# Performance work log

Hardware: AMD Instinct MI355X
Metric: run time of the kernel (lower is better)

Reference implementation:

```python
import jax, jax.numpy as jnp
import numpy as np
from jax import lax

OBS_LEN = 8; FUT_LEN = 12; NC = 2
HT = 32; HG = 32; NZ = 8
G = 1024; P = 64; N = G * P
HPRED = HT + HG + NZ  # 72


def setup_inputs() -> dict:
    key = jax.random.key(0)
    ks = jax.random.split(key, 32)
    f = lambda k, s: jax.random.normal(k, s, dtype=jnp.float32)
    p = lambda k, s: 0.1 * jax.random.normal(k, s, dtype=jnp.float32)
    inp = {
        'obs_traj_rel': f(ks[0], (OBS_LEN, N, NC + 1)),
        'z': f(ks[1], (G, NZ)),
        'traj_h0': f(ks[2], (N, HT)),
        'traj_c0': f(ks[3], (N, HT)),
        'graph_h0': f(ks[4], (N, HG)),
        'graph_c0': f(ks[5], (N, HG)),
        'w_ih_traj': p(ks[6], (4 * HT, NC + 1)),
        'w_hh_traj': p(ks[7], (4 * HT, HT)),
        'b_ih_traj': p(ks[8], (4 * HT,)),
        'b_hh_traj': p(ks[9], (4 * HT,)),
        'gat1_w': p(ks[10], (4, 32, 16)),
        'gat1_asrc': p(ks[11], (4, 16, 1)),
        'gat1_adst': p(ks[12], (4, 16, 1)),
        'gat1_b': jnp.zeros((16,), jnp.float32),
        'gat2_w': p(ks[13], (1, 64, 32)),
        'gat2_asrc': p(ks[14], (1, 32, 1)),
        'gat2_adst': p(ks[15], (1, 32, 1)),
        'gat2_b': jnp.zeros((32,), jnp.float32),
        'w_ih_graph': p(ks[16], (4 * HG, 32)),
        'w_hh_graph': p(ks[17], (4 * HG, HG)),
        'b_ih_graph': p(ks[18], (4 * HG,)),
        'b_hh_graph': p(ks[19], (4 * HG,)),
        'w_ih_pred': p(ks[20], (4 * HPRED, NC)),
        'w_hh_pred': p(ks[21], (4 * HPRED, HPRED)),
        'b_ih_pred': p(ks[22], (4 * HPRED,)),
        'b_hh_pred': p(ks[23], (4 * HPRED,)),
        'w_out': p(ks[24], (NC, HPRED)),
        'b_out': jnp.zeros((NC,), jnp.float32),
        'seq_start_end': jnp.stack([jnp.arange(G) * P, (jnp.arange(G) + 1) * P], axis=1).astype(jnp.int32),
    }
    return inp


def _lstm_cell(x, hc, w_ih, w_hh, b_ih, b_hh):
    h, c = hc
    g = x @ w_ih.T + b_ih + h @ w_hh.T + b_hh
    i, f, gg, o = jnp.split(g, 4, axis=-1)
    c2 = jax.nn.sigmoid(f) * c + jax.nn.sigmoid(i) * jnp.tanh(gg)
    h2 = jax.nn.sigmoid(o) * jnp.tanh(c2)
    return h2, c2


def _inorm(x):  # InstanceNorm1d over node axis: x [T, n, f], normalize over n
    m = x.mean(axis=1, keepdims=True)
    v = x.var(axis=1, keepdims=True)
    return (x - m) * lax.rsqrt(v + 1e-5)


def _gat_layer(x, w, a_src, a_dst, b):
    # x: [T, n, f_in], w: [H, f_in, f_out]
    hp = jnp.einsum('tnf,hfo->thno', x, w)              # [T,H,n,f_out]
    s = jnp.einsum('thno,hoi->thni', hp, a_src)[..., 0]  # [T,H,n]
    d = jnp.einsum('thno,hoi->thni', hp, a_dst)[..., 0]  # [T,H,n]
    attn = s[:, :, :, None] + d[:, :, None, :]           # [T,H,n,n]
    attn = jax.nn.softmax(jax.nn.leaky_relu(attn, 0.2), axis=-1)
    return jnp.einsum('thnm,thmo->thno', attn, hp) + b


def reference(obs_traj_rel, z, traj_h0, traj_c0, graph_h0, graph_c0,
              w_ih_traj, w_hh_traj, b_ih_traj, b_hh_traj,
              gat1_w, gat1_asrc, gat1_adst, gat1_b,
              gat2_w, gat2_asrc, gat2_adst, gat2_b,
              w_ih_graph, w_hh_graph, b_ih_graph, b_hh_graph,
              w_ih_pred, w_hh_pred, b_ih_pred, b_hh_pred,
              w_out, b_out, seq_start_end):
    n_graphs = seq_start_end.shape[0]
    n_total = obs_traj_rel.shape[1]
    peds = n_total // n_graphs  # equal-size subgraphs

    # ---- observation trajectory LSTM ----
    def traj_step(hc, x):
        hc2 = _lstm_cell(x, hc, w_ih_traj, w_hh_traj, b_ih_traj, b_hh_traj)
        return hc2, hc2[0]
    _, traj_hs = lax.scan(traj_step, (traj_h0, traj_c0), obs_traj_rel)  # [T,N,HT]

    # ---- GAT encoder per subgraph (vmapped over equal-size graphs) ----
    def gat_net(x):  # x: [T, peds, 32]
        x = _inorm(x)
        o1 = _gat_layer(x, gat1_w, gat1_asrc, gat1_adst, gat1_b)  # [T,4,n,16]
        t, h, n, fo = o1.shape
        x = jax.nn.elu(jnp.transpose(o1, (0, 2, 1, 3)).reshape(t, n, h * fo))  # [T,n,64]
        x = _inorm(x)
        o2 = _gat_layer(x, gat2_w, gat2_asrc, gat2_adst, gat2_b)  # [T,1,n,32]
        return o2[:, 0]

    xg = traj_hs.reshape(OBS_LEN, n_graphs, peds, HT)
    graph_in = jax.vmap(gat_net, in_axes=1, out_axes=1)(xg)  # [T,G,peds,32]
    graph_in = graph_in.reshape(OBS_LEN, n_total, 32)

    # ---- graph LSTM ----
    def graph_step(hc, x):
        hc2 = _lstm_cell(x, hc, w_ih_graph, w_hh_graph, b_ih_graph, b_hh_graph)
        return hc2, hc2[0]
    _, graph_hs = lax.scan(graph_step, (graph_h0, graph_c0), graph_in)

    # ---- add noise + prediction decoder (eval path, counter=True) ----
    enc = jnp.concatenate([traj_hs[-1], graph_hs[-1]], axis=1)          # [N,64]
    enc_c = jnp.concatenate([jnp.zeros_like(traj_hs[-1]), graph_hs[-1]], axis=1)
    z_rep = jnp.repeat(z, peds, axis=0)                                 # [N,8]
    h = jnp.concatenate([enc, z_rep], axis=1)                           # [N,72]
    h_c = jnp.concatenate([enc_c, z_rep], axis=1)
    c = jnp.zeros_like(h)
    c_c = jnp.zeros_like(h_c)
    out0 = obs_traj_rel[OBS_LEN - 1, :, :NC]

    def dec_step(carry, _):
        h, c, hc_, cc_, out = carry
        h2, c2 = _lstm_cell(out, (h, c), w_ih_pred, w_hh_pred, b_ih_pred, b_hh_pred)
        hc2, cc2 = _lstm_cell(out, (hc_, cc_), w_ih_pred, w_hh_pred, b_ih_pred, b_hh_pred)
        o = (h2 - hc2) @ w_out.T + b_out
        return (h2, c2, hc2, cc2, o), o

    _, preds = lax.scan(dec_step, (h, c, h_c, c_c, out0), None, length=FUT_LEN)
    return preds  # [FUT_LEN, N, 2]
```

## Files before the change

kernel.cpp:

```cpp
#include <hip/hip_runtime.h>


#define OBS 8
#define FUT 12
#define NPED 64
#define HT_ 32
#define HG_ 32
#define NZ_ 8
#define HP_ 72
#define NGR 1024
#define NTOT (NGR * NPED)
#define AP2 80
#define EAP 72

typedef __attribute__((ext_vector_type(8))) short short8_t;
typedef __attribute__((ext_vector_type(4))) float f32x4;
typedef unsigned short u16;

__device__ __forceinline__ float frcp(float x) { return __builtin_amdgcn_rcpf(x); }
__device__ __forceinline__ float sigf(float x) { return frcp(1.0f + __expf(-x)); }
__device__ __forceinline__ float tanh_(float x) {
    float e = __expf(2.0f * x);
    return 1.0f - 2.0f * frcp(e + 1.0f);
}
__device__ __forceinline__ float leaky(float x) { return (x > 0.0f) ? x : 0.2f * x; }
__device__ __forceinline__ u16 bhi(float v) {
    unsigned u = __float_as_uint(v);
    return (u16)((u + 0x7FFFu + ((u >> 16) & 1u)) >> 16);
}
__device__ __forceinline__ float bf2f(u16 h) { return __uint_as_float(((unsigned)h) << 16); }

__global__ __launch_bounds__(512, 1)
void traj_lstm_k(const float* __restrict__ obs,
                 const float* __restrict__ h0,
                 const float* __restrict__ c0,
                 const float* __restrict__ w_ih,
                 const float* __restrict__ w_hh,
                 const float* __restrict__ b_ih,
                 const float* __restrict__ b_hh,
                 float* __restrict__ ws1,
                 float* __restrict__ wsT)
{
    const int g    = blockIdx.x;
    const int lane = threadIdx.x & 63;
    const int wv   = __builtin_amdgcn_readfirstlane((int)(threadIdx.x >> 6));
    const int n    = g * NPED + lane;

    __shared__ __attribute__((aligned(16))) u16 ATh[64 * EAP], ATl[64 * EAP];

    const int pfrag = lane & 15, kg8 = (lane >> 4) * 8;
    const int pcol  = lane & 15;
    const int jg    = wv * 4 + (lane >> 4);

    short8_t wfhT[2], wflT[2];
    {
        int gp = wv * 16 + pfrag, j = gp >> 2, ty = gp & 3, orig = ty * 32 + j;
        #pragma unroll
        for (int kb = 0; kb < 2; ++kb) {
            short8_t fh, fl;
            #pragma unroll
            for (int jj = 0; jj < 8; ++jj) {
                int k = kb * 32 + (lane >> 4) * 8 + jj;
                float v;
                if (k < 32)       v = w_hh[orig * 32 + k];
                else if (k < 35)  v = w_ih[orig * 3 + (k - 32)];
                else if (k == 35) v = b_ih[orig] + b_hh[orig];
                else              v = 0.0f;
                u16 h = bhi(v);
                fh[jj] = (short)h;
                fl[jj] = (short)bhi(v - bf2f(h));
            }
            wfhT[kb] = fh;
            wflT[kb] = fl;
        }
    }
    #pragma unroll
    for (int r = 0; r < 4; ++r) {
        int j = wv * 4 + r;
        float vt = h0[(size_t)n * HT_ + j];
        u16 h = bhi(vt);
        ATh[lane * EAP + j] = h;  ATl[lane * EAP + j] = bhi(vt - bf2f(h));
    }
    if (wv == 0) {
        #pragma unroll
        for (int c = 0; c < 3; ++c) {
            float v = obs[((size_t)0 * NTOT + n) * 3 + c];
            u16 h = bhi(v);
            ATh[lane * EAP + 32 + c] = h;  ATl[lane * EAP + 32 + c] = bhi(v - bf2f(h));
        }
        ATh[lane * EAP + 35] = 0x3F80;  ATl[lane * EAP + 35] = 0;
    } else if (wv == 1) {
        for (int c = 36; c < 64; ++c) { ATh[lane * EAP + c] = 0; ATl[lane * EAP + c] = 0; }
    }
    float cT2[4];
    #pragma unroll
    for (int mb = 0; mb < 4; ++mb)
        cT2[mb] = c0[(size_t)(g * 64 + mb * 16 + pcol) * HT_ + jg];
    __syncthreads();

    for (int t = 0; t < OBS; ++t) {
        float h2[4];
        {
            f32x4 acc[4];
            #pragma unroll
            for (int mb = 0; mb < 4; ++mb) acc[mb] = (f32x4){0.f, 0.f, 0.f, 0.f};
            #pragma unroll
            for (int kb = 0; kb < 2; ++kb) {
                short8_t ah[4], al[4];
                #pragma unroll
                for (int mb = 0; mb < 4; ++mb) {
                    int off = (mb * 16 + pfrag) * EAP + kb * 32 + kg8;
                    ah[mb] = *(const short8_t*)&ATh[off];
                    al[mb] = *(const short8_t*)&ATl[off];
                }
                #pragma unroll
                for (int mb = 0; mb < 4; ++mb) {
                    acc[mb] = __builtin_amdgcn_mfma_f32_16x16x32_bf16(wfhT[kb], ah[mb], acc[mb], 0, 0, 0);
                    acc[mb] = __builtin_amdgcn_mfma_f32_16x16x32_bf16(wflT[kb], ah[mb], acc[mb], 0, 0, 0);
                    acc[mb] = __builtin_amdgcn_mfma_f32_16x16x32_bf16(wfhT[kb], al[mb], acc[mb], 0, 0, 0);
                }
            }
            #pragma unroll
            for (int mb = 0; mb < 4; ++mb) {
                float gi = acc[mb][0], gf = acc[mb][1];
                float gg = acc[mb][2], go = acc[mb][3];
                float c = sigf(gf) * cT2[mb] + sigf(gi) * tanh_(gg);
                cT2[mb] = c;
                h2[mb] = sigf(go) * tanh_(c);
            }
        }
        float sm = (h2[0] + h2[1]) + (h2[2] + h2[3]);
        float sq = (h2[0]*h2[0] + h2[1]*h2[1]) + (h2[2]*h2[2] + h2[3]*h2[3]);
        sm += __shfl_xor(sm, 1);  sq += __shfl_xor(sq, 1);
        sm += __shfl_xor(sm, 2);  sq += __shfl_xor(sq, 2);
        sm += __shfl_xor(sm, 4);  sq += __shfl_xor(sq, 4);
        sm += __shfl_xor(sm, 8);  sq += __shfl_xor(sq, 8);
        float mean = sm * (1.0f / 64.0f);
        float var  = sq * (1.0f / 64.0f) - mean * mean;
        float rstd = rsqrtf(var + 1e-5f);
        __syncthreads();
        #pragma unroll
        for (int mb = 0; mb < 4; ++mb) {
            int p = mb * 16 + pcol;
            u16 h = bhi(h2[mb]);
            ATh[p * EAP + jg] = h;  ATl[p * EAP + jg] = bhi(h2[mb] - bf2f(h));
            ws1[((size_t)t * 32 + jg) * NTOT + g * 64 + p] = (h2[mb] - mean) * rstd;
        }
        if (t == OBS - 1) {
            #pragma unroll
            for (int mb = 0; mb < 4; ++mb)
                wsT[(size_t)jg * NTOT + g * 64 + mb * 16 + pcol] = h2[mb];
        } else if (wv == 0) {
            #pragma unroll
            for (int c = 0; c < 3; ++c) {
                float v = obs[((size_t)(t + 1) * NTOT + n) * 3 + c];
                u16 h = bhi(v);
                ATh[lane * EAP + 32 + c] = h;  ATl[lane * EAP + 32 + c] = bhi(v - bf2f(h));
            }
        }
        __syncthreads();
    }
}

__global__ __launch_bounds__(512, 2)
void gat_k(const float* __restrict__ ws1,
           const float* __restrict__ g1w,
           const float* __restrict__ g1as,
           const float* __restrict__ g1ad,
           const float* __restrict__ g1b,
           const float* __restrict__ g2w,
           const float* __restrict__ g2as,
           const float* __restrict__ g2ad,
           const float* __restrict__ g2b,
           float* __restrict__ ws2)
{
    const int t    = blockIdx.x >> 10;
    const int g    = blockIdx.x & 1023;
    const int lane = threadIdx.x & 63;
    const int wv   = __builtin_amdgcn_readfirstlane((int)(threadIdx.x >> 6));

    __shared__ float hp1s[4096];
    __shared__ float xnx[4096];
    __shared__ float sp1s[512], dp1s[512], sp2s[512], dp2s[512];
    float* xn  = xnx;
    float* x2  = xnx;
    float* hp2 = hp1s;

    #pragma unroll
    for (int r = 0; r < 4; ++r) {
        int f = wv * 4 + r;
        xn[f * 64 + lane] = ws1[((size_t)t * 32 + f) * NTOT + g * 64 + lane];
    }
    __syncthreads();
    {
        const int h_ = wv >> 1;
        const int o0 = (wv & 1) * 8;
        float acc[8];
        #pragma unroll
        for (int q = 0; q < 8; ++q) acc[q] = 0.0f;
        for (int k8 = 0; k8 < 4; ++k8) {
            float xk[8];
            #pragma unroll
            for (int i = 0; i < 8; ++i) xk[i] = xn[(k8 * 8 + i) * 64 + lane];
            #pragma unroll
            for (int i = 0; i < 8; ++i)
                #pragma unroll
                for (int q = 0; q < 8; ++q)
                    acc[q] += g1w[h_ * 512 + (k8 * 8 + i) * 16 + o0 + q] * xk[i];
        }
        float ps = 0.0f, pd = 0.0f;
        #pragma unroll
        for (int q = 0; q < 8; ++q) {
            hp1s[(h_ * 16 + o0 + q) * 64 + lane] = acc[q];
            ps += acc[q] * g1as[h_ * 16 + o0 + q];
            pd += acc[q] * g1ad[h_ * 16 + o0 + q];
        }
        sp1s[((wv & 1) * 4 + h_) * 64 + lane] = ps;
        dp1s[((wv & 1) * 4 + h_) * 64 + lane] = pd;
    }
    __syncthreads();
    {
        const int h_ = wv >> 1;
        const int o0 = (wv & 1) * 8;
        const float sv   = sp1s[h_ * 64 + lane] + sp1s[(4 + h_) * 64 + lane];
        const float dtot = dp1s[h_ * 64 + lane] + dp1s[(4 + h_) * 64 + lane];
        float sum = 0.0f;
        float acc[8];
        #pragma unroll
        for (int q = 0; q < 8; ++q) acc[q] = 0.0f;
        #pragma unroll
        for (int m4 = 0; m4 < 16; ++m4) {
            float e0 = __expf(leaky(sv + __shfl(dtot, m4 * 4 + 0)));
            float e1 = __expf(leaky(sv + __shfl(dtot, m4 * 4 + 1)));
            float e2 = __expf(leaky(sv + __shfl(dtot, m4 * 4 + 2)));
            float e3 = __expf(leaky(sv + __shfl(dtot, m4 * 4 + 3)));
            sum += e0 + e1 + e2 + e3;
            #pragma unroll
            for (int q = 0; q < 8; ++q) {
                float4 hv = *reinterpret_cast<const float4*>(&hp1s[(h_ * 16 + o0 + q) * 64 + m4 * 4]);
                acc[q] += e0 * hv.x + e1 * hv.y + e2 * hv.z + e3 * hv.w;
            }
        }
        float rs = frcp(sum);
        #pragma unroll
        for (int q = 0; q < 8; ++q) {
            float v = acc[q] * rs + g1b[o0 + q];
            v = (v > 0.0f) ? v : (__expf(v) - 1.0f);
            float sm = v, sq = v * v;
            #pragma unroll
            for (int m = 1; m < 64; m <<= 1) { sm += __shfl_xor(sm, m); sq += __shfl_xor(sq, m); }
            float mean = sm * (1.0f / 64.0f);
            float var  = sq * (1.0f / 64.0f) - mean * mean;
            x2[(h_ * 16 + o0 + q) * 64 + lane] = (v - mean) * rsqrtf(var + 1e-5f);
        }
    }
    __syncthreads();
    {
        float acc[4];
        #pragma unroll
        for (int q = 0; q < 4; ++q) acc[q] = 0.0f;
        for (int k8 = 0; k8 < 8; ++k8) {
            float xk[8];
            #pragma unroll
            for (int i = 0; i < 8; ++i) xk[i] = x2[(k8 * 8 + i) * 64 + lane];
            #pragma unroll
            for (int i = 0; i < 8; ++i)
                #pragma unroll
                for (int q = 0; q < 4; ++q)
                    acc[q] += g2w[(k8 * 8 + i) * 32 + wv * 4 + q] * xk[i];
        }
        float ps = 0.0f, pd = 0.0f;
        #pragma unroll
        for (int q = 0; q < 4; ++q) {
            hp2[(wv * 4 + q) * 64 + lane] = acc[q];
            ps += acc[q] * g2as[wv * 4 + q];
            pd += acc[q] * g2ad[wv * 4 + q];
        }
        sp2s[wv * 64 + lane] = ps;
        dp2s[wv * 64 + lane] = pd;
    }
    __syncthreads();
    {
        float sv = 0.0f, dtot = 0.0f;
        #pragma unroll
        for (int w = 0; w < 8; ++w) { sv += sp2s[w * 64 + lane]; dtot += dp2s[w * 64 + lane]; }
        float sum = 0.0f;
        float acc[4];
        #pragma unroll
        for (int q = 0; q < 4; ++q) acc[q] = 0.0f;
        #pragma unroll
        for (int m4 = 0; m4 < 16; ++m4) {
            float e0 = __expf(leaky(sv + __shfl(dtot, m4 * 4 + 0)));
            float e1 = __expf(leaky(sv + __shfl(dtot, m4 * 4 + 1)));
            float e2 = __expf(leaky(sv + __shfl(dtot, m4 * 4 + 2)));
            float e3 = __expf(leaky(sv + __shfl(dtot, m4 * 4 + 3)));
            sum += e0 + e1 + e2 + e3;
            #pragma unroll
            for (int q = 0; q < 4; ++q) {
                float4 hv = *reinterpret_cast<const float4*>(&hp2[(wv * 4 + q) * 64 + m4 * 4]);
                acc[q] += e0 * hv.x + e1 * hv.y + e2 * hv.z + e3 * hv.w;
            }
        }
        float rs = frcp(sum);
        #pragma unroll
        for (int q = 0; q < 4; ++q)
            ws2[((size_t)t * 32 + wv * 4 + q) * NTOT + g * 64 + lane] = acc[q] * rs + g2b[wv * 4 + q];
    }
}

__global__ __launch_bounds__(512, 1)
void graph_lstm_k(const float* __restrict__ ws2,
                  const float* __restrict__ graph_h0,
                  const float* __restrict__ graph_c0,
                  const float* __restrict__ w_ih_g,
                  const float* __restrict__ w_hh_g,
                  const float* __restrict__ b_ih_g,
                  const float* __restrict__ b_hh_g,
                  float* __restrict__ wsG)
{
    const int g    = blockIdx.x;
    const int lane = threadIdx.x & 63;
    const int wv   = __builtin_amdgcn_readfirstlane((int)(threadIdx.x >> 6));
    const int n    = g * NPED + lane;

    __shared__ __attribute__((aligned(16))) u16 AGh[64 * EAP], AGl[64 * EAP];
    __shared__ float biasg[128];

    const int pfrag = lane & 15, kg8 = (lane >> 4) * 8;
    const int pcol = lane & 15;
    const int jg   = wv * 4 + (lane >> 4);

    short8_t wfhG[2], wflG[2];
    {
        int gp = wv * 16 + pfrag, j = gp >> 2, ty = gp & 3, orig = ty * 32 + j;
        #pragma unroll
        for (int kb = 0; kb < 2; ++kb) {
            short8_t fhG, flG;
            #pragma unroll
            for (int jj = 0; jj < 8; ++jj) {
                int k = kb * 32 + (lane >> 4) * 8 + jj;
                float vG = (k < 32) ? w_ih_g[orig * 32 + k] : w_hh_g[orig * 32 + (k - 32)];
                u16 hG = bhi(vG); fhG[jj] = (short)hG; flG[jj] = (short)bhi(vG - bf2f(hG));
            }
            wfhG[kb] = fhG; wflG[kb] = flG;
        }
    }
    #pragma unroll
    for (int r = 0; r < 4; ++r) {
        int j = wv * 4 + r;
        float vg = graph_h0[(size_t)n * HG_ + j];
        u16 hg = bhi(vg);
        AGh[lane * EAP + 32 + j] = hg;  AGl[lane * EAP + 32 + j] = bhi(vg - bf2f(hg));
    }
    float cG2[4];
    #pragma unroll
    for (int mb = 0; mb < 4; ++mb)
        cG2[mb] = graph_c0[(size_t)(g * 64 + mb * 16 + pcol) * HG_ + jg];
    if (threadIdx.x < 128) biasg[threadIdx.x] = b_ih_g[threadIdx.x] + b_hh_g[threadIdx.x];

    for (int t = 0; t < OBS; ++t) {
        #pragma unroll
        for (int r = 0; r < 4; ++r) {
            int f = wv * 4 + r;
            float v = ws2[((size_t)t * 32 + f) * NTOT + g * 64 + lane];
            u16 h = bhi(v);
            AGh[lane * EAP + f] = h;  AGl[lane * EAP + f] = bhi(v - bf2f(h));
        }
        __syncthreads();
        float h2G[4];
        {
            f32x4 acc[4];
            #pragma unroll
            for (int mb = 0; mb < 4; ++mb) acc[mb] = (f32x4){0.f, 0.f, 0.f, 0.f};
            #pragma unroll
            for (int kb = 0; kb < 2; ++kb) {
                short8_t ah[4], al[4];
                #pragma unroll
                for (int mb = 0; mb < 4; ++mb) {
                    int off = (mb * 16 + pfrag) * EAP + kb * 32 + kg8;
                    ah[mb] = *(const short8_t*)&AGh[off];
                    al[mb] = *(const short8_t*)&AGl[off];
                }
                #pragma unroll
                for (int mb = 0; mb < 4; ++mb) {
                    acc[mb] = __builtin_amdgcn_mfma_f32_16x16x32_bf16(wfhG[kb], ah[mb], acc[mb], 0, 0, 0);
                    acc[mb] = __builtin_amdgcn_mfma_f32_16x16x32_bf16(wflG[kb], ah[mb], acc[mb], 0, 0, 0);
                    acc[mb] = __builtin_amdgcn_mfma_f32_16x16x32_bf16(wfhG[kb], al[mb], acc[mb], 0, 0, 0);
                }
            }
            const float bI = biasg[jg], bF = biasg[32 + jg], bG = biasg[64 + jg], bO = biasg[96 + jg];
            #pragma unroll
            for (int mb = 0; mb < 4; ++mb) {
                float gi = acc[mb][0] + bI, gf = acc[mb][1] + bF;
                float gg = acc[mb][2] + bG, go = acc[mb][3] + bO;
                float c = sigf(gf) * cG2[mb] + sigf(gi) * tanh_(gg);
                cG2[mb] = c;
                h2G[mb] = sigf(go) * tanh_(c);
            }
        }
        __syncthreads();
        #pragma unroll
        for (int mb = 0; mb < 4; ++mb) {
            int p = mb * 16 + pcol;
            u16 h = bhi(h2G[mb]);
            AGh[p * EAP + 32 + jg] = h;  AGl[p * EAP + 32 + jg] = bhi(h2G[mb] - bf2f(h));
        }
        if (t == OBS - 1) {
            #pragma unroll
            for (int mb = 0; mb < 4; ++mb)
                wsG[(size_t)jg * NTOT + g * 64 + mb * 16 + pcol] = h2G[mb];
        }
    }
}

__global__ __launch_bounds__(512, 1)
void stgat_dec(const float* __restrict__ obs,
               const float* __restrict__ zin,
               const float* __restrict__ w_ih_p,
               const float* __restrict__ w_hh_p,
               const float* __restrict__ b_ih_p,
               const float* __restrict__ b_hh_p,
               const float* __restrict__ w_out,
               const float* __restrict__ b_out,
               const float* __restrict__ wsT,
               const float* __restrict__ wsG,
               float* __restrict__ out)
{
    const int g    = blockIdx.x;
    const int lane = threadIdx.x & 63;
    const int wv   = __builtin_amdgcn_readfirstlane((int)(threadIdx.x >> 6));
    const int n    = g * NPED + lane;

    __shared__ __attribute__((aligned(16))) u16 Apk[2 * 64 * AP2 + 16];
    __shared__ __attribute__((aligned(16))) short8_t WloS[18 * 3 * 64];
    __shared__ float red0[512], red1[512];
    u16* AhiA = Apk;
    u16* AhiB = Apk + 64 * AP2;

    const int pfrag = lane & 15, kgrp = (lane >> 4) * 8;
    const int pcol  = lane & 15;
    const int mb2   = wv & 3;
    const int nb2   = 16 + (wv >> 2);

    short8_t wfh[3][3];
    {
        const int col = lane & 15, lb = lane >> 4;
        #pragma unroll
        for (int s = 0; s < 3; ++s) {
            int nb = (s == 2) ? nb2 : (wv + 8 * s);
            int gp = nb * 16 + col;
            int j = gp >> 2, ty = gp & 3;
            int orig = ty * HP_ + j;
            #pragma unroll
            for (int kb = 0; kb < 3; ++kb) {
                short8_t fh, fl;
                #pragma unroll
                for (int jj = 0; jj < 8; ++jj) {
                    int k = kb * 32 + lb * 8 + jj;
                    float v;
                    if (k < 72)       v = w_hh_p[orig * HP_ + k];
                    else if (k == 72) v = w_ih_p[orig * 2 + 0];
                    else if (k == 73) v = w_ih_p[orig * 2 + 1];
                    else if (k == 74) v = b_ih_p[orig] + b_hh_p[orig];
                    else              v = 0.0f;
                    u16 hb = bhi(v);
                    fh[jj] = (short)hb;
                    fl[jj] = (short)bhi(v - bf2f(hb));
                }
                wfh[s][kb] = fh;
                if (s < 2 || (wv & 3) == 0)
                    WloS[(nb * 3 + kb) * 64 + lane] = fl;
            }
        }
    }
    float wo0[3], wo1[3];
    #pragma unroll
    for (int s = 0; s < 3; ++s) {
        int nb = (s == 2) ? nb2 : (wv + 8 * s);
        int j = nb * 4 + (lane >> 4);
        wo0[s] = w_out[j];
        wo1[s] = w_out[HP_ + j];
    }
    const float bo0 = b_out[0], bo1 = b_out[1];

    {
        float px0 = obs[(7 * NTOT + n) * 3 + 0];
        float px1 = obs[(7 * NTOT + n) * 3 + 1];
        #pragma unroll
        for (int kk = 0; kk < 12; ++kk) {
            int k = wv + kk * 8;
            if (k < AP2) {
                float va, vb;
                if (k < 32)       { va = wsT[(size_t)k * NTOT + n];            vb = 0.0f; }
                else if (k < 64)  { va = vb = wsG[(size_t)(k - 32) * NTOT + n]; }
                else if (k < 72)  { va = vb = zin[g * NZ_ + (k - 64)]; }
                else if (k == 72) { va = vb = px0; }
                else if (k == 73) { va = vb = px1; }
                else if (k == 74) { va = vb = 1.0f; }
                else              { va = vb = 0.0f; }
                AhiA[lane * AP2 + k] = bhi(va);
                AhiB[lane * AP2 + k] = bhi(vb);
            }
        }
        if (wv == 0 && lane < 16) Apk[2 * 64 * AP2 + lane] = 0;
    }
    __syncthreads();

    float cstA[2][4], cstB[2][4], cstA2 = 0.f, cstB2 = 0.f;
    #pragma unroll
    for (int s = 0; s < 2; ++s)
        #pragma unroll
        for (int mb = 0; mb < 4; ++mb) { cstA[s][mb] = 0.0f; cstB[s][mb] = 0.0f; }

    for (int st = 0; st < FUT; ++st) {
        float h2A[2][4], h2B[2][4], h2A2, h2B2;
        {
            f32x4 acc[2][4];
            f32x4 acc2 = (f32x4){0.f, 0.f, 0.f, 0.f};
            #pragma unroll
            for (int s = 0; s < 2; ++s)
                #pragma unroll
                for (int mb = 0; mb < 4; ++mb) acc[s][mb] = (f32x4){0.f, 0.f, 0.f, 0.f};
            #pragma unroll
            for (int kb = 0; kb < 3; ++kb) {
                short8_t ah[4];
                #pragma unroll
                for (int mb = 0; mb < 4; ++mb) {
                    int off = (mb * 16 + pfrag) * AP2 + kb * 32 + kgrp;
                    ah[mb] = *(const short8_t*)&AhiA[off];
                }
                #pragma unroll
                for (int s = 0; s < 2; ++s) {
                    int nb = wv + 8 * s;
                    short8_t wl = WloS[(nb * 3 + kb) * 64 + lane];
                    #pragma unroll
                    for (int mb = 0; mb < 4; ++mb) {
                        acc[s][mb] = __builtin_amdgcn_mfma_f32_16x16x32_bf16(wfh[s][kb], ah[mb], acc[s][mb], 0, 0, 0);
                        acc[s][mb] = __builtin_amdgcn_mfma_f32_16x16x32_bf16(wl,         ah[mb], acc[s][mb], 0, 0, 0);
                    }
                }
                short8_t ah2 = *(const short8_t*)&AhiA[(mb2 * 16 + pfrag) * AP2 + kb * 32 + kgrp];
                short8_t wl2 = WloS[(nb2 * 3 + kb) * 64 + lane];
                acc2 = __builtin_amdgcn_mfma_f32_16x16x32_bf16(wfh[2][kb], ah2, acc2, 0, 0, 0);
                acc2 = __builtin_amdgcn_mfma_f32_16x16x32_bf16(wl2,        ah2, acc2, 0, 0, 0);
            }
            #pragma unroll
            for (int s = 0; s < 2; ++s)
                #pragma unroll
                for (int mb = 0; mb < 4; ++mb) {
                    float gi = acc[s][mb][0], gf = acc[s][mb][1];
                    float gg = acc[s][mb][2], go = acc[s][mb][3];
                    float c = sigf(gf) * cstA[s][mb] + sigf(gi) * tanh_(gg);
                    cstA[s][mb] = c;
                    h2A[s][mb] = sigf(go) * tanh_(c);
                }
            {
                float gi = acc2[0], gf = acc2[1], gg = acc2[2], go = acc2[3];
                float c = sigf(gf) * cstA2 + sigf(gi) * tanh_(gg);
                cstA2 = c;
                h2A2 = sigf(go) * tanh_(c);
            }
        }
        {
            f32x4 acc[2][4];
            f32x4 acc2 = (f32x4){0.f, 0.f, 0.f, 0.f};
            #pragma unroll
            for (int s = 0; s < 2; ++s)
                #pragma unroll
                for (int mb = 0; mb < 4; ++mb) acc[s][mb] = (f32x4){0.f, 0.f, 0.f, 0.f};
            #pragma unroll
            for (int kb = 0; kb < 3; ++kb) {
                short8_t bh[4];
                #pragma unroll
                for (int mb = 0; mb < 4; ++mb) {
                    int off = (mb * 16 + pfrag) * AP2 + kb * 32 + kgrp;
                    bh[mb] = *(const short8_t*)&AhiB[off];
                }
                #pragma unroll
                for (int s = 0; s < 2; ++s) {
                    int nb = wv + 8 * s;
                    short8_t wl = WloS[(nb * 3 + kb) * 64 + lane];
                    #pragma unroll
                    for (int mb = 0; mb < 4; ++mb) {
                        acc[s][mb] = __builtin_amdgcn_mfma_f32_16x16x32_bf16(wfh[s][kb], bh[mb], acc[s][mb], 0, 0, 0);
                        acc[s][mb] = __builtin_amdgcn_mfma_f32_16x16x32_bf16(wl,         bh[mb], acc[s][mb], 0, 0, 0);
                    }
                }
                short8_t bh2 = *(const short8_t*)&AhiB[(mb2 * 16 + pfrag) * AP2 + kb * 32 + kgrp];
                short8_t wl2 = WloS[(nb2 * 3 + kb) * 64 + lane];
                acc2 = __builtin_amdgcn_mfma_f32_16x16x32_bf16(wfh[2][kb], bh2, acc2, 0, 0, 0);
                acc2 = __builtin_amdgcn_mfma_f32_16x16x32_bf16(wl2,        bh2, acc2, 0, 0, 0);
            }
            #pragma unroll
            for (int s = 0; s < 2; ++s)
                #pragma unroll
                for (int mb = 0; mb < 4; ++mb) {
                    float gi = acc[s][mb][0], gf = acc[s][mb][1];
                    float gg = acc[s][mb][2], go = acc[s][mb][3];
                    float c = sigf(gf) * cstB[s][mb] + sigf(gi) * tanh_(gg);
                    cstB[s][mb] = c;
                    h2B[s][mb] = sigf(go) * tanh_(c);
                }
            {
                float gi = acc2[0], gf = acc2[1], gg = acc2[2], go = acc2[3];
                float c = sigf(gf) * cstB2 + sigf(gi) * tanh_(gg);
                cstB2 = c;
                h2B2 = sigf(go) * tanh_(c);
            }
        }
        float po0[4] = {0.f, 0.f, 0.f, 0.f}, po1[4] = {0.f, 0.f, 0.f, 0.f};
        #pragma unroll
        for (int s = 0; s < 2; ++s)
            #pragma unroll
            for (int mb = 0; mb < 4; ++mb) {
                float dh = h2A[s][mb] - h2B[s][mb];
                po0[mb] += wo0[s] * dh;
                po1[mb] += wo1[s] * dh;
            }
        {
            float dh2 = h2A2 - h2B2;
            float c0 = wo0[2] * dh2, c1 = wo1[2] * dh2;
            #pragma unroll
            for (int mb = 0; mb < 4; ++mb) {
                po0[mb] += (mb == mb2) ? c0 : 0.0f;
                po1[mb] += (mb == mb2) ? c1 : 0.0f;
            }
        }
        #pragma unroll
        for (int mb = 0; mb < 4; ++mb) {
            po0[mb] += __shfl_xor(po0[mb], 16);  po0[mb] += __shfl_xor(po0[mb], 32);
            po1[mb] += __shfl_xor(po1[mb], 16);  po1[mb] += __shfl_xor(po1[mb], 32);
        }
        if ((lane >> 4) == 0) {
            #pragma unroll
            for (int mb = 0; mb < 4; ++mb) {
                red0[wv * 64 + mb * 16 + lane] = po0[mb];
                red1[wv * 64 + mb * 16 + lane] = po1[mb];
            }
        }
        __syncthreads();
        #pragma unroll
        for (int s = 0; s < 2; ++s) {
            int j = (wv + 8 * s) * 4 + (lane >> 4);
            #pragma unroll
            for (int mb = 0; mb < 4; ++mb) {
                int p = mb * 16 + pcol;
                AhiA[p * AP2 + j] = bhi(h2A[s][mb]);
                AhiB[p * AP2 + j] = bhi(h2B[s][mb]);
            }
        }
        {
            int j2 = nb2 * 4 + (lane >> 4);
            int p2 = mb2 * 16 + pcol;
            AhiA[p2 * AP2 + j2] = bhi(h2A2);
            AhiB[p2 * AP2 + j2] = bhi(h2B2);
        }
        if (wv == 0) {
            float o0 = bo0, o1 = bo1;
            #pragma unroll
            for (int w = 0; w < 8; ++w) { o0 += red0[w * 64 + lane]; o1 += red1[w * 64 + lane]; }
            *reinterpret_cast<float2*>(&out[(size_t)(st * NTOT + n) * 2]) = make_float2(o0, o1);
            u16 h0_ = bhi(o0);
            u16 h1  = bhi(o1);
            AhiA[lane * AP2 + 72] = h0_;  AhiB[lane * AP2 + 72] = h0_;
            AhiA[lane * AP2 + 73] = h1;   AhiB[lane * AP2 + 73] = h1;
        }
        __syncthreads();
    }
}

extern "C" void kernel_launch(void* const* d_in, const int* in_sizes, int n_in,
                              void* d_out, int out_size, void* d_ws, size_t ws_size,
                              hipStream_t stream) {
    (void)in_sizes; (void)n_in; (void)out_size; (void)ws_size;
    const size_t NF = (size_t)OBS * 32 * NTOT;
    float* ws1 = (float*)d_ws;
    float* ws2 = ws1 + NF;
    float* wsT = ws2 + NF;
    float* wsG = wsT + (size_t)32 * NTOT;

    traj_lstm_k<<<dim3(NGR), dim3(512), 0, stream>>>(
        (const float*)d_in[0], (const float*)d_in[2], (const float*)d_in[3],
        (const float*)d_in[6], (const float*)d_in[7], (const float*)d_in[8], (const float*)d_in[9],
        ws1, wsT);

    gat_k<<<dim3(OBS * NGR), dim3(512), 0, stream>>>(
        ws1,
        (const float*)d_in[10], (const float*)d_in[11], (const float*)d_in[12], (const float*)d_in[13],
        (const float*)d_in[14], (const float*)d_in[15], (const float*)d_in[16], (const float*)d_in[17],
        ws2);

    graph_lstm_k<<<dim3(NGR), dim3(512), 0, stream>>>(
        ws2, (const float*)d_in[4], (const float*)d_in[5],
        (const float*)d_in[18], (const float*)d_in[19], (const float*)d_in[20], (const float*)d_in[21],
        wsG);

    stgat_dec<<<dim3(NGR), dim3(512), 0, stream>>>(
        (const float*)d_in[0], (const float*)d_in[1],
        (const float*)d_in[22], (const float*)d_in[23],
        (const float*)d_in[24], (const float*)d_in[25],
        (const float*)d_in[26], (const float*)d_in[27],
        wsT, wsG, (float*)d_out);
}
```

Before: 651.6 us.

## Use split-bf16 MFMA for GAT projections and share layer-2 attention weights

Replaces the scalar FMA loops for both GAT linear projections with bf16 MFMA 16x16x32. Each float operand is split into high and low bf16 parts and three products are summed to approximate fp32 accuracy. Inputs are stored transposed in padded LDS so MFMA fragments can be loaded directly. Layer-2 attention exponentials are now computed once per block into a shared LDS matrix instead of being recomputed by all 8 waves. In exchange the kernel uses more LDS and adds a barrier, and precision differs slightly from pure fp32.

```diff
diff --git a/kernel.cpp b/kernel.cpp
--- a/kernel.cpp
+++ b/kernel.cpp
@@ -12,6 +12,9 @@
 #define NTOT (NGR * NPED)
 #define AP2 80
 #define EAP 72
+#define XNP 56
+#define X2P 72
+#define P2P 68
 
 typedef __attribute__((ext_vector_type(8))) short short8_t;
 typedef __attribute__((ext_vector_type(4))) float f32x4;
@@ -179,51 +182,86 @@
     const int lane = threadIdx.x & 63;
     const int wv   = __builtin_amdgcn_readfirstlane((int)(threadIdx.x >> 6));
 
-    __shared__ float hp1s[4096];
-    __shared__ float xnx[4096];
-    __shared__ float sp1s[512], dp1s[512], sp2s[512], dp2s[512];
-    float* xn  = xnx;
-    float* x2  = xnx;
+    __shared__ __attribute__((aligned(16))) u16 xnh[64 * XNP], xnl[64 * XNP];
+    __shared__ float hp1s[64 * 64];
+    __shared__ __attribute__((aligned(16))) u16 x2h[64 * X2P], x2l[64 * X2P];
+    __shared__ __attribute__((aligned(16))) float P2[64 * P2P];
+    __shared__ float s1f[256], d1f[256];
+    __shared__ float sp2f[128], dp2f[128];
     float* hp2 = hp1s;
+
+    const int pfrag = lane & 15, kg8 = (lane >> 4) * 8;
+
+    const int mb1 = wv >> 1;
+    const int nb1 = (wv & 1) * 2;
+    short8_t w1h, w1l;
+    {
+        short8_t fh, fl;
+        #pragma unroll
+        for (int j = 0; j < 8; ++j) {
+            int k = kg8 + j;
+            float v = g1w[mb1 * 512 + k * 16 + pfrag];
+            u16 h = bhi(v);
+            fh[j] = (short)h;
+            fl[j] = (short)bhi(v - bf2f(h));
+        }
+        w1h = fh; w1l = fl;
+    }
+    const int mb2g = wv >> 2, nb2g = wv & 3;
+    short8_t w2h[2], w2l[2];
+    #pragma unroll
+    for (int kb = 0; kb < 2; ++kb) {
+        short8_t fh, fl;
+        #pragma unroll
+        for (int j = 0; j < 8; ++j) {
+            int k = kb * 32 + kg8 + j;
+            float v = g2w[k * 32 + mb2g * 16 + pfrag];
+            u16 h = bhi(v);
+            fh[j] = (short)h;
+            fl[j] = (short)bhi(v - bf2f(h));
+        }
+        w2h[kb] = fh; w2l[kb] = fl;
+    }
 
     #pragma unroll
     for (int r = 0; r < 4; ++r) {
         int f = wv * 4 + r;
-        xn[f * 64 + lane] = ws1[((size_t)t * 32 + f) * NTOT + g * 64 + lane];
+        float v = ws1[((size_t)t * 32 + f) * NTOT + g * 64 + lane];
+        u16 h = bhi(v);
+        xnh[lane * XNP + f] = h;
+        xnl[lane * XNP + f] = bhi(v - bf2f(h));
     }
     __syncthreads();
+
+    #pragma unroll
+    for (int nbi = 0; nbi < 2; ++nbi) {
+        int nb = nb1 + nbi;
+        short8_t bh = *(const short8_t*)&xnh[(nb * 16 + pfrag) * XNP + kg8];
+        short8_t bl = *(const short8_t*)&xnl[(nb * 16 + pfrag) * XNP + kg8];
+        f32x4 acc = (f32x4){0.f, 0.f, 0.f, 0.f};
+        acc = __builtin_amdgcn_mfma_f32_16x16x32_bf16(w1h, bh, acc, 0, 0, 0);
+        acc = __builtin_amdgcn_mfma_f32_16x16x32_bf16(w1l, bh, acc, 0, 0, 0);
+        acc = __builtin_amdgcn_mfma_f32_16x16x32_bf16(w1h, bl, acc, 0, 0, 0);
+        float sp = 0.0f, dp = 0.0f;
+        #pragma unroll
+        for (int reg = 0; reg < 4; ++reg) {
+            int o_in = (lane >> 4) * 4 + reg;
+            hp1s[(mb1 * 16 + o_in) * 64 + nb * 16 + pfrag] = acc[reg];
+            sp += acc[reg] * g1as[mb1 * 16 + o_in];
+            dp += acc[reg] * g1ad[mb1 * 16 + o_in];
+        }
+        sp += __shfl_xor(sp, 16);  sp += __shfl_xor(sp, 32);
+        dp += __shfl_xor(dp, 16);  dp += __shfl_xor(dp, 32);
+        s1f[mb1 * 64 + nb * 16 + pfrag] = sp;
+        d1f[mb1 * 64 + nb * 16 + pfrag] = dp;
+    }
+    __syncthreads();
+
     {
         const int h_ = wv >> 1;
         const int o0 = (wv & 1) * 8;
-        float acc[8];
-        #pragma unroll
-        for (int q = 0; q < 8; ++q) acc[q] = 0.0f;
-        for (int k8 = 0; k8 < 4; ++k8) {
-            float xk[8];
-            #pragma unroll
-            for (int i = 0; i < 8; ++i) xk[i] = xn[(k8 * 8 + i) * 64 + lane];
-            #pragma unroll
-            for (int i = 0; i < 8; ++i)
-                #pragma unroll
-                for (int q = 0; q < 8; ++q)
-                    acc[q] += g1w[h_ * 512 + (k8 * 8 + i) * 16 + o0 + q] * xk[i];
-        }
-        float ps = 0.0f, pd = 0.0f;
-        #pragma unroll
-        for (int q = 0; q < 8; ++q) {
-            hp1s[(h_ * 16 + o0 + q) * 64 + lane] = acc[q];
-            ps += acc[q] * g1as[h_ * 16 + o0 + q];
-            pd += acc[q] * g1ad[h_ * 16 + o0 + q];
-        }
-        sp1s[((wv & 1) * 4 + h_) * 64 + lane] = ps;
-        dp1s[((wv & 1) * 4 + h_) * 64 + lane] = pd;
-    }
-    __syncthreads();
-    {
-        const int h_ = wv >> 1;
-        const int o0 = (wv & 1) * 8;
-        const float sv   = sp1s[h_ * 64 + lane] + sp1s[(4 + h_) * 64 + lane];
-        const float dtot = dp1s[h_ * 64 + lane] + dp1s[(4 + h_) * 64 + lane];
+        const float sv   = s1f[h_ * 64 + lane];
+        const float dtot = d1f[h_ * 64 + lane];
         float sum = 0.0f;
         float acc[8];
         #pragma unroll
@@ -251,54 +289,67 @@
             for (int m = 1; m < 64; m <<= 1) { sm += __shfl_xor(sm, m); sq += __shfl_xor(sq, m); }
             float mean = sm * (1.0f / 64.0f);
             float var  = sq * (1.0f / 64.0f) - mean * mean;
-            x2[(h_ * 16 + o0 + q) * 64 + lane] = (v - mean) * rsqrtf(var + 1e-5f);
+            float vn = (v - mean) * rsqrtf(var + 1e-5f);
+            int f = h_ * 16 + o0 + q;
+            u16 hh = bhi(vn);
+            x2h[lane * X2P + f] = hh;
+            x2l[lane * X2P + f] = bhi(vn - bf2f(hh));
         }
     }
     __syncthreads();
-    {
-        float acc[4];
-        #pragma unroll
-        for (int q = 0; q < 4; ++q) acc[q] = 0.0f;
-        for (int k8 = 0; k8 < 8; ++k8) {
-            float xk[8];
-            #pragma unroll
-            for (int i = 0; i < 8; ++i) xk[i] = x2[(k8 * 8 + i) * 64 + lane];
-            #pragma unroll
-            for (int i = 0; i < 8; ++i)
-                #pragma unroll
-                for (int q = 0; q < 4; ++q)
-                    acc[q] += g2w[(k8 * 8 + i) * 32 + wv * 4 + q] * xk[i];
-        }
-        float ps = 0.0f, pd = 0.0f;
-        #pragma unroll
-        for (int q = 0; q < 4; ++q) {
-            hp2[(wv * 4 + q) * 64 + lane] = acc[q];
-            ps += acc[q] * g2as[wv * 4 + q];
-            pd += acc[q] * g2ad[wv * 4 + q];
-        }
-        sp2s[wv * 64 + lane] = ps;
-        dp2s[wv * 64 + lane] = pd;
+
+    {
+        f32x4 acc = (f32x4){0.f, 0.f, 0.f, 0.f};
+        #pragma unroll
+        for (int kb = 0; kb < 2; ++kb) {
+            short8_t bh = *(const short8_t*)&x2h[(nb2g * 16 + pfrag) * X2P + kb * 32 + kg8];
+            short8_t bl = *(const short8_t*)&x2l[(nb2g * 16 + pfrag) * X2P + kb * 32 + kg8];
+            acc = __builtin_amdgcn_mfma_f32_16x16x32_bf16(w2h[kb], bh, acc, 0, 0, 0);
+            acc = __builtin_amdgcn_mfma_f32_16x16x32_bf16(w2l[kb], bh, acc, 0, 0, 0);
+            acc = __builtin_amdgcn_mfma_f32_16x16x32_bf16(w2h[kb], bl, acc, 0, 0, 0);
+        }
+        float sp = 0.0f, dp = 0.0f;
+        #pragma unroll
+        for (int reg = 0; reg < 4; ++reg) {
+            int o_all = mb2g * 16 + (lane >> 4) * 4 + reg;
+            hp2[o_all * 64 + nb2g * 16 + pfrag] = acc[reg];
+            sp += acc[reg] * g2as[o_all];
+            dp += acc[reg] * g2ad[o_all];
+        }
+        sp += __shfl_xor(sp, 16);  sp += __shfl_xor(sp, 32);
+        dp += __shfl_xor(dp, 16);  dp += __shfl_xor(dp, 32);
+        sp2f[mb2g * 64 + nb2g * 16 + pfrag] = sp;
+        dp2f[mb2g * 64 + nb2g * 16 + pfrag] = dp;
     }
     __syncthreads();
-    {
-        float sv = 0.0f, dtot = 0.0f;
-        #pragma unroll
-        for (int w = 0; w < 8; ++w) { sv += sp2s[w * 64 + lane]; dtot += dp2s[w * 64 + lane]; }
+
+    const float sv2 = sp2f[lane] + sp2f[64 + lane];
+    const float dt2 = dp2f[lane] + dp2f[64 + lane];
+    {
+        float e[8];
+        #pragma unroll
+        for (int k = 0; k < 8; ++k) {
+            float dm = __shfl(dt2, wv * 8 + k);
+            e[k] = __expf(leaky(sv2 + dm));
+        }
+        *reinterpret_cast<float4*>(&P2[lane * P2P + wv * 8 + 0]) = make_float4(e[0], e[1], e[2], e[3]);
+        *reinterpret_cast<float4*>(&P2[lane * P2P + wv * 8 + 4]) = make_float4(e[4], e[5], e[6], e[7]);
+    }
+    __syncthreads();
+
+    {
         float sum = 0.0f;
         float acc[4];
         #pragma unroll
         for (int q = 0; q < 4; ++q) acc[q] = 0.0f;
         #pragma unroll
         for (int m4 = 0; m4 < 16; ++m4) {
-            float e0 = __expf(leaky(sv + __shfl(dtot, m4 * 4 + 0)));
-            float e1 = __expf(leaky(sv + __shfl(dtot, m4 * 4 + 1)));
-            float e2 = __expf(leaky(sv + __shfl(dtot, m4 * 4 + 2)));
-            float e3 = __expf(leaky(sv + __shfl(dtot, m4 * 4 + 3)));
-            sum += e0 + e1 + e2 + e3;
+            float4 pv = *reinterpret_cast<const float4*>(&P2[lane * P2P + m4 * 4]);
+            sum += (pv.x + pv.y) + (pv.z + pv.w);
             #pragma unroll
             for (int q = 0; q < 4; ++q) {
                 float4 hv = *reinterpret_cast<const float4*>(&hp2[(wv * 4 + q) * 64 + m4 * 4]);
-                acc[q] += e0 * hv.x + e1 * hv.y + e2 * hv.z + e3 * hv.w;
+                acc[q] += pv.x * hv.x + pv.y * hv.y + pv.z * hv.z + pv.w * hv.w;
             }
         }
         float rs = frcp(sum);
```

Result: slower. 853.4 us (+31.0%).
